# Optimization experiments

Measured on AMD Instinct MI355X. Metric: run time of the kernel, lower is better.

Reference implementation:

```python
import jax, jax.numpy as jnp
import numpy as np

EMBED_DIM = 1024
NUM_HEADS = 16
HEAD_DIM = EMBED_DIM // NUM_HEADS


def _sinusoid_pos_emb(seq_len, dim):
    pos = jnp.arange(seq_len, dtype=jnp.float32)
    idx = jnp.arange(dim // 2, dtype=jnp.float32)
    inv_freq = 1.0 / (10000.0 ** (2.0 * idx / dim))
    ang = pos[:, None] * inv_freq[None, :]          # [S, D/2]
    return jnp.concatenate([jnp.sin(ang), jnp.cos(ang)], axis=-1)  # [S, D]


def _relative_shift(x):
    # x: [B, H, S, S] -> Transformer-XL shift
    b, h, s, _ = x.shape
    x = jnp.pad(x, ((0, 0), (0, 0), (0, 0), (1, 0)))
    x = x.reshape(b, h, s + 1, s)
    return x[:, :, 1:, :].reshape(b, h, s, s)


def setup_inputs() -> dict:
    key = jax.random.key(0)
    ks = jax.random.split(key, 12)
    D = EMBED_DIM
    sc = 1.0 / np.sqrt(D)
    inp = {"x": jax.random.normal(ks[0], (2, 2048, D), dtype=jnp.float32)}
    for i, name in enumerate(["Wq", "Wk", "Wv", "Wp", "Wo"]):
        inp[name] = jax.random.normal(ks[1 + i], (D, D), dtype=jnp.float32) * sc
        inp["b" + name[1].lower()] = jnp.zeros((D,), dtype=jnp.float32)
    inp["u"] = jax.random.normal(ks[6], (1, NUM_HEADS, 1, HEAD_DIM), dtype=jnp.float32) * 0.05
    inp["v"] = jax.random.normal(ks[7], (1, NUM_HEADS, 1, HEAD_DIM), dtype=jnp.float32) * 0.05
    return inp


def reference(x, Wq, bq, Wk, bk, Wv, bv, Wp, bp, Wo, bo, u, v):
    B, S, D = x.shape
    H, P = NUM_HEADS, HEAD_DIM

    def heads(t):  # [B,S,D] -> [B,H,S,P]
        return t.reshape(B, S, H, P).transpose(0, 2, 1, 3)

    q = heads(x @ Wq + bq)
    k = heads(x @ Wk + bk)
    val = heads(x @ Wv + bv)

    pos = _sinusoid_pos_emb(S, D) @ Wp + bp            # [S, D]
    pos = pos.reshape(S, H, P).transpose(1, 0, 2)       # [H, S, P]

    content_score = jnp.einsum('bhsp,bhtp->bhst', q + u, k)
    pos_score = jnp.einsum('bhsp,htp->bhst', q + v, pos)
    pos_score = _relative_shift(pos_score)

    score = (content_score + pos_score) / jnp.sqrt(jnp.float32(P))
    weights = jax.nn.softmax(score, axis=-1)            # dropout = 0 (inference)
    out = jnp.einsum('bhst,bhtp->bhsp', weights, val)
    out = out.transpose(0, 2, 1, 3).reshape(B, S, D)
    return out @ Wo + bo
```

## Files before the change

kernel.cpp:

```cpp
#include <hip/hip_runtime.h>
#include <hip/hip_bf16.h>

typedef unsigned short u16;
typedef unsigned int u32;
typedef __bf16 bf16x8 __attribute__((ext_vector_type(8)));
typedef float f32x4 __attribute__((ext_vector_type(4)));

#define SEQ 2048
#define NH 16
#define PD 64
#define DM 1024

#if __has_builtin(__builtin_amdgcn_exp2f)
#define EXP2(x) __builtin_amdgcn_exp2f(x)
#else
#define EXP2(x) __expf((x) * 0.6931471805599453f)
#endif

__device__ __forceinline__ float bf2f(u16 s) {
  u32 t = ((u32)s) << 16;
  float f;
  __builtin_memcpy(&f, &t, 4);
  return f;
}
__device__ __forceinline__ u16 f2bf(float f) {
  u32 x;
  __builtin_memcpy(&x, &f, 4);
  x = (x + 0x7fffu + ((x >> 16) & 1u)) >> 16;
  return (u16)x;
}
__device__ __forceinline__ u32 pack2(float a, float b) {
  __hip_bfloat162 h = __float22bfloat162_rn(float2{a, b});
  u32 r;
  __builtin_memcpy(&r, &h, 4);
  return r;
}
__device__ __forceinline__ void gld16(const u16* g, u16* l) {
  __builtin_amdgcn_global_load_lds(
      (const __attribute__((address_space(1))) unsigned int*)(g),
      (__attribute__((address_space(3))) unsigned int*)(l), 16, 0, 0);
}

struct PrepArgs {
  const void* x;
  const void* w0; const void* w1; const void* w2; const void* w3; const void* w4;
  const void* p0; const void* p1; const void* p2; const void* p3; const void* p4;
  const void* p5; const void* p6;
};

__global__ __launch_bounds__(256) void prep_kernel(PrepArgs pa,
                                                   u16* __restrict__ xb,
                                                   u16* __restrict__ sinb,
                                                   u16* __restrict__ WT,
                                                   float* __restrict__ pf,
                                                   int* __restrict__ flag) {
  __shared__ int sz[256], sh[256];
  __shared__ u16 t[64][72];
  int tid = threadIdx.x;

  {
    const u16* probe = (const u16*)pa.w0;
    int zeros = 0, huge = 0;
    for (int j = 0; j < 16; ++j) {
      int i = tid * 16 + j;
      u16 v = probe[i];
      int e = (v >> 7) & 0xFF;
      if (((i & 1) == 0) && v == 0) zeros++;
      if (e >= 0x8C) huge++;
    }
    sz[tid] = zeros; sh[tid] = huge;
    __syncthreads();
    for (int s = 128; s > 0; s >>= 1) {
      if (tid < s) { sz[tid] += sz[tid + s]; sh[tid] += sh[tid + s]; }
      __syncthreads();
    }
  }
  int f = (sz[0] > 1024 || sh[0] > 200) ? 1 : 0;
  int id = blockIdx.x;
  if (id == 0 && tid == 0) *flag = f;

  if (id < 4096) {
    int i = (id * 256 + tid) * 4;
    if (f) {
      float4 fv = *(const float4*)((const float*)pa.x + i);
      u16 o[4] __attribute__((aligned(8))) = {f2bf(fv.x), f2bf(fv.y), f2bf(fv.z), f2bf(fv.w)};
      *(uint2*)(xb + i) = *(const uint2*)o;
    } else {
      *(uint2*)(xb + i) = *(const uint2*)((const u16*)pa.x + i);
    }
  } else if (id < 6144) {
    int base = ((id - 4096) * 256 + tid) * 4;
    u16 o[4] __attribute__((aligned(8)));
#pragma unroll
    for (int e = 0; e < 4; ++e) {
      int idx = base + e;
      int s = idx >> 10;
      int i = idx & 1023;
      int j = i & 511;
      float invf = __expf(-(float)j * (9.210340371976184f / 512.0f));
      float ang = (float)s * invf;
      float val = (i < 512) ? __sinf(ang) : __cosf(ang);
      o[e] = f2bf(val);
    }
    *(uint2*)(sinb + base) = *(const uint2*)o;
  } else if (id < 7424) {
    int tt = id - 6144;
    int z = tt >> 8;
    int rem = tt & 255;
    const void* src = (z == 0) ? pa.w0 : (z == 1) ? pa.w1 : (z == 2) ? pa.w2
                     : (z == 3) ? pa.w3 : pa.w4;
    u16* out = WT + (size_t)z * DM * DM;
    int r0 = (rem >> 4) * 64, c0 = (rem & 15) * 64;
    int tr = tid >> 2;
    int tc = (tid & 3) * 16;
    if (f) {
      const float* g = (const float*)src + (size_t)(r0 + tr) * DM + c0 + tc;
#pragma unroll
      for (int q = 0; q < 4; ++q) {
        float4 fv = *(const float4*)(g + q * 4);
        t[tr][tc + q * 4 + 0] = f2bf(fv.x);
        t[tr][tc + q * 4 + 1] = f2bf(fv.y);
        t[tr][tc + q * 4 + 2] = f2bf(fv.z);
        t[tr][tc + q * 4 + 3] = f2bf(fv.w);
      }
    } else {
      const uint4* g = (const uint4*)((const u16*)src + (size_t)(r0 + tr) * DM + c0 + tc);
      uint4 a = g[0], bb = g[1];
      *(uint4*)&t[tr][tc] = a;
      *(uint4*)&t[tr][tc + 8] = bb;
    }
    __syncthreads();
    u16 tmp[16] __attribute__((aligned(16)));
#pragma unroll
    for (int jj = 0; jj < 16; ++jj) tmp[jj] = t[tc + jj][tr];
    uint4* o = (uint4*)(out + (size_t)(c0 + tr) * DM + r0 + tc);
    o[0] = *(const uint4*)&tmp[0];
    o[1] = *(const uint4*)&tmp[8];
  } else {
    int idx = (id - 7424) * 256 + tid;
    int seg = idx >> 10, off = idx & 1023;
    const void* s = (seg == 0) ? pa.p0 : (seg == 1) ? pa.p1 : (seg == 2) ? pa.p2
                   : (seg == 3) ? pa.p3 : (seg == 4) ? pa.p4 : (seg == 5) ? pa.p5 : pa.p6;
    pf[idx] = f ? ((const float*)s)[off] : bf2f(((const u16*)s)[off]);
  }
}

struct GemmArgs {
  const u16* A;  const u16* A3;
  const u16* Bt0; const u16* Bt1; const u16* Bt2; const u16* Bt3;
  const float* b0; const float* b1; const float* b2; const float* b3;
  void* C0; void* C1; void* C2; void* C3;
  int N, K, M3;
  const int* flag; int outFp32; int vtrans;
};

__global__ __launch_bounds__(256, 4) void gemm_bt_kernel(GemmArgs p) {
  __shared__ u16 As[128 * 64];
  __shared__ u16 Bs[128 * 64];
  int z = blockIdx.z;
  if (z == 3 && (int)blockIdx.y * 128 >= p.M3) return;
  const u16* A = (z == 3) ? p.A3 : p.A;
  const u16* Bt = (z == 0) ? p.Bt0 : (z == 1) ? p.Bt1 : (z == 2) ? p.Bt2 : p.Bt3;
  const float* bias = (z == 0) ? p.b0 : (z == 1) ? p.b1 : (z == 2) ? p.b2 : p.b3;
  void* Cv = (z == 0) ? p.C0 : (z == 1) ? p.C1 : (z == 2) ? p.C2 : p.C3;
  int K = p.K, N = p.N;
  bool f32o = p.outFp32 && (*p.flag);
  bool vt = p.vtrans && (z == 2);

  int tid = threadIdx.x;
  int wave = tid >> 6, lane = tid & 63;
  int quad = lane >> 4, l16 = lane & 15;
  int m0 = blockIdx.y * 128, n0 = blockIdx.x * 128;
  int wm = (wave >> 1) * 64, wn = (wave & 1) * 64;

  int trow = tid >> 2;
  int tcol = ((tid & 3) ^ ((tid >> 3) & 3)) * 8;
  const u16* ga = A + (size_t)(m0 + trow) * K + tcol;
  const u16* gb = Bt + (size_t)(n0 + trow) * K + tcol;
  u16* lwa = As + wave * 512;
  u16* lwb = Bs + wave * 512;
  int slotx = (quad ^ ((l16 >> 1) & 3)) * 8;

  f32x4 acc[4][4] = {};

  for (int k0 = 0; k0 < K; k0 += 64) {
    __syncthreads();
    gld16(ga + k0, lwa);
    gld16(ga + (size_t)64 * K + k0, lwa + 2048);
    gld16(ga + k0 + 32, lwa + 4096);
    gld16(ga + (size_t)64 * K + k0 + 32, lwa + 6144);
    gld16(gb + k0, lwb);
    gld16(gb + (size_t)64 * K + k0, lwb + 2048);
    gld16(gb + k0 + 32, lwb + 4096);
    gld16(gb + (size_t)64 * K + k0 + 32, lwb + 6144);
    __syncthreads();
#pragma unroll
    for (int kh = 0; kh < 2; ++kh) {
      int kbase = kh * 4096;
      bf16x8 af[4], bfv[4];
#pragma unroll
      for (int i = 0; i < 4; ++i) {
        af[i] = *(const bf16x8*)&As[kbase + (wm + i * 16 + l16) * 32 + slotx];
        bfv[i] = *(const bf16x8*)&Bs[kbase + (wn + i * 16 + l16) * 32 + slotx];
      }
#pragma unroll
      for (int tm = 0; tm < 4; ++tm)
#pragma unroll
        for (int tn = 0; tn < 4; ++tn)
          acc[tm][tn] = __builtin_amdgcn_mfma_f32_16x16x32_bf16(af[tm], bfv[tn], acc[tm][tn], 0, 0, 0);
    }
  }

#pragma unroll
  for (int tm = 0; tm < 4; ++tm) {
    int row = m0 + wm + tm * 16 + quad * 4;
#pragma unroll
    for (int tn = 0; tn < 4; ++tn) {
      int col = n0 + wn + tn * 16 + l16;
      float bv = bias[col];
      if (vt) {
        u16 o4[4] __attribute__((aligned(8)));
#pragma unroll
        for (int r = 0; r < 4; ++r) o4[r] = f2bf(acc[tm][tn][r] + bv);
        int bq_ = row >> 11, s = row & 2047;
        *(uint2*)((u16*)Cv + ((size_t)(bq_ * 1024 + col)) * 2048 + s) = *(const uint2*)o4;
      } else {
#pragma unroll
        for (int r = 0; r < 4; ++r) {
          float val = acc[tm][tn][r] + bv;
          if (f32o) ((float*)Cv)[(size_t)(row + r) * N + col] = val;
          else ((u16*)Cv)[(size_t)(row + r) * N + col] = f2bf(val);
        }
      }
    }
  }
}

__global__ __launch_bounds__(256, 4) void attn_kernel(
    const u16* __restrict__ Q, const u16* __restrict__ Kg,
    const u16* __restrict__ Vtg, const u16* __restrict__ Rg,
    const float* __restrict__ pf,
    u16* __restrict__ O) {
  __shared__ __align__(16) u16 KP[64 * 72];
  __shared__ __align__(16) u16 RVs[4096];
  __shared__ __align__(16) u16 Bb[128 * 66];

  int tid = threadIdx.x, wave = tid >> 6, lane = tid & 63;
  int quad = lane >> 4, l16 = lane & 15;
  int id = blockIdx.x;
  int bh = (id & 7) + ((id >> 8) << 3);
  int s0 = ((id >> 3) & 31) * 64;
  int b = bh >> 4, h = bh & 15;
  const float* pu = pf + 5 * 1024 + h * PD;
  const float* pv = pf + 6 * 1024 + h * PD;

  int arow = wave * 16 + l16;
  int sl_base = wave * 16 + quad * 4;

  int srow = wave * 16 + (lane >> 2);
  int scol = ((lane & 3) ^ ((lane >> 3) & 3)) * 8;
  u16* kbase = KP + wave * 512;
  u16* rvbase = RVs + wave * 512;
  int kb0 = l16 * 32 + (quad ^ ((l16 >> 1) & 3)) * 8;

  const float QS = 0.18033688011112042f;
  bf16x8 qu0, qu1, qv0a, qv1a, qv0b, qv1b;
  {
    const u16* qp = Q + ((size_t)(b * SEQ + s0 + arow)) * DM + h * PD;
    int row2 = s0 + arow + 1;
    if (row2 > SEQ - 1) row2 = SEQ - 1;
    const u16* qp2 = Q + ((size_t)(b * SEQ + row2)) * DM + h * PD;
    u16 qa[16] __attribute__((aligned(16)));
    u16 qb[16] __attribute__((aligned(16)));
    *(uint4*)&qa[0] = *(const uint4*)(qp + quad * 8);
    *(uint4*)&qa[8] = *(const uint4*)(qp + 32 + quad * 8);
    *(uint4*)&qb[0] = *(const uint4*)(qp2 + quad * 8);
    *(uint4*)&qb[8] = *(const uint4*)(qp2 + 32 + quad * 8);
    u16 fu[16] __attribute__((aligned(16)));
    u16 fv0[16] __attribute__((aligned(16)));
    u16 fv1[16] __attribute__((aligned(16)));
#pragma unroll
    for (int j = 0; j < 8; ++j) {
      float u0 = pu[quad * 8 + j], u1 = pu[32 + quad * 8 + j];
      float v0 = pv[quad * 8 + j], v1 = pv[32 + quad * 8 + j];
      fu[j] = f2bf((bf2f(qa[j]) + u0) * QS);
      fu[8 + j] = f2bf((bf2f(qa[8 + j]) + u1) * QS);
      fv0[j] = f2bf((bf2f(qa[j]) + v0) * QS);
      fv0[8 + j] = f2bf((bf2f(qa[8 + j]) + v1) * QS);
      fv1[j] = f2bf((bf2f(qb[j]) + v0) * QS);
      fv1[8 + j] = f2bf((bf2f(qb[8 + j]) + v1) * QS);
    }
    __builtin_memcpy(&qu0, &fu[0], 16);
    __builtin_memcpy(&qu1, &fu[8], 16);
    __builtin_memcpy(&qv0a, &fv0[0], 16);
    __builtin_memcpy(&qv1a, &fv0[8], 16);
    __builtin_memcpy(&qv0b, &fv1[0], 16);
    __builtin_memcpy(&qv1b, &fv1[8], 16);
  }

  bf16x8 onesf;
  {
    u16 onearr[8] __attribute__((aligned(16)));
#pragma unroll
    for (int j = 0; j < 8; ++j) onearr[j] = 0x3F80;
    __builtin_memcpy(&onesf, onearr, 16);
  }

  auto dmaR = [&](int tb0) {
    int tg = tb0 + srow;
    tg = tg < 0 ? 0 : (tg > SEQ - 1 ? SEQ - 1 : tg);
    const u16* gr = Rg + (size_t)tg * DM + h * PD + scol;
    gld16(gr, rvbase);
    gld16(gr + 32, rvbase + 2048);
  };
  auto slice = [&](bf16x8 fa0, bf16x8 fa1, int slotBase, int rowOff, int lo, int hi) {
#pragma unroll
    for (int tt = 0; tt < 4; ++tt) {
      f32x4 pacc = {};
      bf16x8 b0 = *(const bf16x8*)&RVs[kb0 + tt * 512];
      bf16x8 b1 = *(const bf16x8*)&RVs[kb0 + tt * 512 + 2048];
      pacc = __builtin_amdgcn_mfma_f32_16x16x32_bf16(fa0, b0, pacc, 0, 0, 0);
      pacc = __builtin_amdgcn_mfma_f32_16x16x32_bf16(fa1, b1, pacc, 0, 0, 0);
      int rloc = tt * 16 + l16;
      bool ok = (rloc >= lo) & (rloc <= hi);
      u32 w0 = ok ? pack2(pacc[0], pacc[1]) : 0u;
      u32 w1 = ok ? pack2(pacc[2], pacc[3]) : 0u;
      int prow = (slotBase + rloc + rowOff) & 127;
      *(u32*)&Bb[prow * 66 + sl_base] = w0;
      *(u32*)&Bb[prow * 66 + sl_base + 2] = w1;
    }
  };

  f32x4 lacc = {};
  f32x4 oacc[4] = {};

  dmaR(SEQ - 65 - s0);
  __syncthreads();
  slice(qv0a, qv1a, 0, 0, 0, 63);

  for (int j0 = 0; j0 < SEQ; j0 += 64) {
    int a1 = (j0 >> 6) + 1;
    int slot = (a1 & 1) << 6;
    bool p0n = (j0 <= s0);
    bool p1n = (j0 >= s0);
    __syncthreads();
    {
      const u16* gk = Kg + (size_t)(b * SEQ + j0 + srow) * DM + h * PD + scol;
      gld16(gk, kbase);
      gld16(gk + 32, kbase + 2048);
    }
    dmaR((p0n ? (SEQ - 65 - s0) : (-65 - s0)) + 64 * a1);
    __syncthreads();

    f32x4 acc[4];
#pragma unroll
    for (int tn = 0; tn < 4; ++tn) {
      f32x4 a = {};
      bf16x8 b0 = *(const bf16x8*)&KP[kb0 + tn * 512];
      bf16x8 b1 = *(const bf16x8*)&KP[kb0 + tn * 512 + 2048];
      a = __builtin_amdgcn_mfma_f32_16x16x32_bf16(qu0, b0, a, 0, 0, 0);
      a = __builtin_amdgcn_mfma_f32_16x16x32_bf16(qu1, b1, a, 0, 0, 0);
      acc[tn] = a;
    }

    if (p0n) slice(qv0a, qv1a, slot, 0, 0, s0 + 64 - 64 * a1);
    if (p0n && p1n) {
      __syncthreads();
      dmaR(64 * a1 - s0 - 65);
      __syncthreads();
    }
    if (p1n) slice(qv0b, qv1b, slot, 1, s0 + 65 - 64 * a1, 63);
    __syncthreads();

    {
      const u16* gv = Vtg + ((size_t)(b * NH + h) * PD + srow) * SEQ + j0 + scol;
      gld16(gv, rvbase);
      gld16(gv + 32, rvbase + 2048);
    }

    int g0 = l16 - sl_base + 64 + j0;
#pragma unroll
    for (int tn = 0; tn < 4; ++tn) {
#pragma unroll
      for (int r = 0; r < 4; ++r) {
        int rl = (g0 + tn * 16 - r) & 127;
        acc[tn][r] += bf2f(Bb[rl * 66 + sl_base + r]);
      }
    }

#pragma unroll
    for (int r = 0; r < 4; ++r) {
      u32 w0 = pack2(EXP2(acc[0][r]), EXP2(acc[1][r]));
      u32 w1 = pack2(EXP2(acc[2][r]), EXP2(acc[3][r]));
      u16 ec[4] = {(u16)w0, (u16)(w0 >> 16), (u16)w1, (u16)(w1 >> 16)};
      int row = sl_base + r;
      u16* prow_ = KP + row * 72 + l16;
#pragma unroll
      for (int cr = 0; cr < 4; ++cr) {
        int c = (cr + quad) & 3;
        prow_[c * 16] = ec[c];
      }
    }
    __syncthreads();

    {
      bf16x8 pa0 = *(const bf16x8*)&KP[arow * 72 + quad * 8];
      bf16x8 pa1 = *(const bf16x8*)&KP[arow * 72 + 32 + quad * 8];
      lacc = __builtin_amdgcn_mfma_f32_16x16x32_bf16(pa0, onesf, lacc, 0, 0, 0);
      lacc = __builtin_amdgcn_mfma_f32_16x16x32_bf16(pa1, onesf, lacc, 0, 0, 0);
#pragma unroll
      for (int tp = 0; tp < 4; ++tp) {
        bf16x8 b0 = *(const bf16x8*)&RVs[kb0 + tp * 512];
        bf16x8 b1 = *(const bf16x8*)&RVs[kb0 + tp * 512 + 2048];
        oacc[tp] = __builtin_amdgcn_mfma_f32_16x16x32_bf16(pa0, b0, oacc[tp], 0, 0, 0);
        oacc[tp] = __builtin_amdgcn_mfma_f32_16x16x32_bf16(pa1, b1, oacc[tp], 0, 0, 0);
      }
    }
  }

  float li[4];
#pragma unroll
  for (int r = 0; r < 4; ++r) li[r] = 1.f / lacc[r];
#pragma unroll
  for (int tp = 0; tp < 4; ++tp) {
    int pcol = tp * 16 + l16;
#pragma unroll
    for (int r = 0; r < 4; ++r) {
      int sg = s0 + sl_base + r;
      O[((size_t)(b * SEQ + sg)) * DM + h * PD + pcol] = f2bf(oacc[tp][r] * li[r]);
    }
  }
}

extern "C" void kernel_launch(void* const* d_in, const int* in_sizes, int n_in,
                              void* d_out, int out_size, void* d_ws, size_t ws_size,
                              hipStream_t stream) {
  (void)in_sizes; (void)n_in; (void)out_size; (void)ws_size;
  const void* x  = d_in[0];
  const void* Wq = d_in[1];
  const void* bq = d_in[2];
  const void* Wk = d_in[3];
  const void* bk = d_in[4];
  const void* Wv = d_in[5];
  const void* bv = d_in[6];
  const void* Wp = d_in[7];
  const void* bp = d_in[8];
  const void* Wo = d_in[9];
  const void* bo = d_in[10];
  const void* u  = d_in[11];
  const void* v  = d_in[12];

  char* base = (char*)d_ws;
  int* flag = (int*)base;
  float* pf = (float*)(base + 64);
  u16* wbase = (u16*)(base + 64 + 7168 * 4);
  u16* WT   = wbase;
  u16* xb   = WT + (size_t)5 * DM * DM;
  u16* sinb = xb + (size_t)2 * SEQ * DM;
  u16* Qb   = sinb + (size_t)SEQ * DM;
  u16* Kb   = Qb + (size_t)2 * SEQ * DM;
  u16* Vtb  = Kb + (size_t)2 * SEQ * DM;
  u16* Rb   = Vtb + (size_t)2 * SEQ * DM;
  u16* Ab   = xb;

  PrepArgs pa;
  pa.x = x;
  pa.w0 = Wq; pa.w1 = Wk; pa.w2 = Wv; pa.w3 = Wp; pa.w4 = Wo;
  pa.p0 = bq; pa.p1 = bk; pa.p2 = bv; pa.p3 = bp; pa.p4 = bo; pa.p5 = u; pa.p6 = v;
  prep_kernel<<<7452, 256, 0, stream>>>(pa, xb, sinb, WT, pf, flag);

  GemmArgs qkv;
  qkv.A = xb; qkv.A3 = sinb;
  qkv.Bt0 = WT; qkv.Bt1 = WT + (size_t)DM * DM; qkv.Bt2 = WT + (size_t)2 * DM * DM;
  qkv.Bt3 = WT + (size_t)3 * DM * DM;
  qkv.b0 = pf; qkv.b1 = pf + 1024; qkv.b2 = pf + 2048; qkv.b3 = pf + 3072;
  qkv.C0 = Qb; qkv.C1 = Kb; qkv.C2 = Vtb; qkv.C3 = Rb;
  qkv.N = DM; qkv.K = DM; qkv.M3 = SEQ; qkv.flag = flag; qkv.outFp32 = 0; qkv.vtrans = 1;
  gemm_bt_kernel<<<dim3(8, 32, 4), 256, 0, stream>>>(qkv);

  attn_kernel<<<dim3(1024), 256, 0, stream>>>(Qb, Kb, Vtb, Rb, pf, Ab);

  GemmArgs fo;
  fo.A = Ab; fo.A3 = Ab;
  fo.Bt0 = WT + (size_t)4 * DM * DM; fo.Bt1 = fo.Bt0; fo.Bt2 = fo.Bt0; fo.Bt3 = fo.Bt0;
  fo.b0 = pf + 4096; fo.b1 = fo.b0; fo.b2 = fo.b0; fo.b3 = fo.b0;
  fo.C0 = d_out; fo.C1 = d_out; fo.C2 = d_out; fo.C3 = d_out;
  fo.N = DM; fo.K = DM; fo.M3 = 0; fo.flag = flag; fo.outFp32 = 1; fo.vtrans = 0;
  gemm_bt_kernel<<<dim3(8, 32, 1), 256, 0, stream>>>(fo);
}
```

Measured before the change: 290.5 us.

## Fuse Q/K/V projections into one kernel sharing the x tile across three weights

Replaces the generic batched GEMM launch for the Q, K, V and positional projections with a dedicated kernel. Each block loads one 128x32 tile of x and reuses it against three weight tiles, so x is read once for all three projections. The positional projection runs as separate blocks of the same grid. The per-thread accumulator count triples in the QKV path, which raises register pressure (launch bounds lowered to 3), and the tiles are narrower (64 columns, K step 32), which may reduce efficiency per block.

After: 284.5 us. 2.0% less time.

```diff
diff --git a/kernel.cpp b/kernel.cpp
--- a/kernel.cpp
+++ b/kernel.cpp
@@ -142,6 +142,110 @@
     const void* s = (seg == 0) ? pa.p0 : (seg == 1) ? pa.p1 : (seg == 2) ? pa.p2
                    : (seg == 3) ? pa.p3 : (seg == 4) ? pa.p4 : (seg == 5) ? pa.p5 : pa.p6;
     pf[idx] = f ? ((const float*)s)[off] : bf2f(((const u16*)s)[off]);
+  }
+}
+
+__global__ __launch_bounds__(256, 3) void qkv_kernel(
+    const u16* __restrict__ xb, const u16* __restrict__ sinb,
+    const u16* __restrict__ WT, const float* __restrict__ pf,
+    u16* __restrict__ Qb, u16* __restrict__ Kb, u16* __restrict__ Vtb,
+    u16* __restrict__ Rb) {
+  __shared__ u16 As[128 * 32];
+  __shared__ u16 Bs[3 * 64 * 32];
+  int tid = threadIdx.x;
+  int wave = tid >> 6, lane = tid & 63;
+  int quad = lane >> 4, l16 = lane & 15;
+  int bx = blockIdx.x, by = blockIdx.y;
+  bool isR = by >= 32;
+  int m0 = (isR ? (by - 32) : by) * 128;
+  int n0 = bx * 64;
+  int wm = (wave >> 1) * 64, wn = (wave & 1) * 32;
+
+  int trow = tid >> 2;
+  int tcol = ((tid & 3) ^ ((tid >> 3) & 3)) * 8;
+  const u16* A = isR ? sinb : xb;
+  const u16* ga = A + (size_t)(m0 + trow) * DM + tcol;
+  const u16* gb = WT + (isR ? (size_t)3 * DM * DM : 0) + (size_t)(n0 + trow) * DM + tcol;
+  u16* lwa = As + wave * 512;
+  u16* lwb = Bs + wave * 512;
+  int slotx = (quad ^ ((l16 >> 1) & 3)) * 8;
+
+  if (!isR) {
+    f32x4 acc[3][4][2] = {};
+    for (int k0 = 0; k0 < DM; k0 += 32) {
+      __syncthreads();
+      gld16(ga + k0, lwa);
+      gld16(ga + (size_t)64 * DM + k0, lwa + 2048);
+      gld16(gb + k0, lwb);
+      gld16(gb + (size_t)DM * DM + k0, lwb + 2048);
+      gld16(gb + (size_t)2 * DM * DM + k0, lwb + 4096);
+      __syncthreads();
+      bf16x8 af[4];
+#pragma unroll
+      for (int i = 0; i < 4; ++i)
+        af[i] = *(const bf16x8*)&As[(wm + i * 16 + l16) * 32 + slotx];
+#pragma unroll
+      for (int z = 0; z < 3; ++z) {
+        bf16x8 b0 = *(const bf16x8*)&Bs[z * 2048 + (wn + l16) * 32 + slotx];
+        bf16x8 b1 = *(const bf16x8*)&Bs[z * 2048 + (wn + 16 + l16) * 32 + slotx];
+#pragma unroll
+        for (int tm = 0; tm < 4; ++tm) {
+          acc[z][tm][0] = __builtin_amdgcn_mfma_f32_16x16x32_bf16(af[tm], b0, acc[z][tm][0], 0, 0, 0);
+          acc[z][tm][1] = __builtin_amdgcn_mfma_f32_16x16x32_bf16(af[tm], b1, acc[z][tm][1], 0, 0, 0);
+        }
+      }
+    }
+#pragma unroll
+    for (int tm = 0; tm < 4; ++tm) {
+      int row = m0 + wm + tm * 16 + quad * 4;
+#pragma unroll
+      for (int tn = 0; tn < 2; ++tn) {
+        int col = n0 + wn + tn * 16 + l16;
+        float bq = pf[col], bk = pf[1024 + col], bv = pf[2048 + col];
+#pragma unroll
+        for (int r = 0; r < 4; ++r) {
+          Qb[(size_t)(row + r) * DM + col] = f2bf(acc[0][tm][tn][r] + bq);
+          Kb[(size_t)(row + r) * DM + col] = f2bf(acc[1][tm][tn][r] + bk);
+        }
+        u16 o4[4] __attribute__((aligned(8)));
+#pragma unroll
+        for (int r = 0; r < 4; ++r) o4[r] = f2bf(acc[2][tm][tn][r] + bv);
+        int bq_ = row >> 11, s = row & 2047;
+        *(uint2*)(Vtb + ((size_t)(bq_ * 1024 + col)) * 2048 + s) = *(const uint2*)o4;
+      }
+    }
+  } else {
+    f32x4 acc[4][2] = {};
+    for (int k0 = 0; k0 < DM; k0 += 32) {
+      __syncthreads();
+      gld16(ga + k0, lwa);
+      gld16(ga + (size_t)64 * DM + k0, lwa + 2048);
+      gld16(gb + k0, lwb);
+      __syncthreads();
+      bf16x8 af[4];
+#pragma unroll
+      for (int i = 0; i < 4; ++i)
+        af[i] = *(const bf16x8*)&As[(wm + i * 16 + l16) * 32 + slotx];
+      bf16x8 b0 = *(const bf16x8*)&Bs[(wn + l16) * 32 + slotx];
+      bf16x8 b1 = *(const bf16x8*)&Bs[(wn + 16 + l16) * 32 + slotx];
+#pragma unroll
+      for (int tm = 0; tm < 4; ++tm) {
+        acc[tm][0] = __builtin_amdgcn_mfma_f32_16x16x32_bf16(af[tm], b0, acc[tm][0], 0, 0, 0);
+        acc[tm][1] = __builtin_amdgcn_mfma_f32_16x16x32_bf16(af[tm], b1, acc[tm][1], 0, 0, 0);
+      }
+    }
+#pragma unroll
+    for (int tm = 0; tm < 4; ++tm) {
+      int row = m0 + wm + tm * 16 + quad * 4;
+#pragma unroll
+      for (int tn = 0; tn < 2; ++tn) {
+        int col = n0 + wn + tn * 16 + l16;
+        float br = pf[3072 + col];
+#pragma unroll
+        for (int r = 0; r < 4; ++r)
+          Rb[(size_t)(row + r) * DM + col] = f2bf(acc[tm][tn][r] + br);
+      }
+    }
   }
 }
 
@@ -469,14 +573,7 @@
   pa.p0 = bq; pa.p1 = bk; pa.p2 = bv; pa.p3 = bp; pa.p4 = bo; pa.p5 = u; pa.p6 = v;
   prep_kernel<<<7452, 256, 0, stream>>>(pa, xb, sinb, WT, pf, flag);
 
-  GemmArgs qkv;
-  qkv.A = xb; qkv.A3 = sinb;
-  qkv.Bt0 = WT; qkv.Bt1 = WT + (size_t)DM * DM; qkv.Bt2 = WT + (size_t)2 * DM * DM;
-  qkv.Bt3 = WT + (size_t)3 * DM * DM;
-  qkv.b0 = pf; qkv.b1 = pf + 1024; qkv.b2 = pf + 2048; qkv.b3 = pf + 3072;
-  qkv.C0 = Qb; qkv.C1 = Kb; qkv.C2 = Vtb; qkv.C3 = Rb;
-  qkv.N = DM; qkv.K = DM; qkv.M3 = SEQ; qkv.flag = flag; qkv.outFp32 = 0; qkv.vtrans = 1;
-  gemm_bt_kernel<<<dim3(8, 32, 4), 256, 0, stream>>>(qkv);
+  qkv_kernel<<<dim3(16, 48), 256, 0, stream>>>(xb, sinb, WT, pf, Qb, Kb, Vtb, Rb);
 
   attn_kernel<<<dim3(1024), 256, 0, stream>>>(Qb, Kb, Vtb, Rb, pf, Ab);
 
```
